# Kernel tuning notes

Hardware: AMD Instinct MI355X
Metric: run time of the kernel (lower is better)

Reference implementation:

```python
import jax, jax.numpy as jnp
import numpy as np

N = 50000          # nodes
E = 800000         # edges (before self-loops)
IN_CH = 128
HID = 64
HEADS = 4
OUT_CH = 16
NEG_SLOPE = 0.2    # PyG GATConv default leaky_relu slope
EPS = 1e-16        # PyG softmax denominator epsilon


def glorot(key, shape):
    fan_in, fan_out = shape[0], shape[-1]
    lim = np.sqrt(6.0 / (fan_in + fan_out))
    return jax.random.uniform(key, shape, jnp.float32, -lim, lim)


def setup_inputs() -> dict:
    key = jax.random.key(0)
    ks = jax.random.split(key, 12)
    x = jax.random.normal(ks[0], (N, IN_CH), jnp.float32)
    edge_index = jax.random.randint(ks[1], (2, E), 0, N, jnp.int32)
    # layer 1: in -> HID per head, HEADS heads
    W1 = glorot(ks[2], (IN_CH, HEADS * HID))
    a_src1 = glorot(ks[3], (HEADS, HID))
    a_dst1 = glorot(ks[4], (HEADS, HID))
    b1 = jnp.zeros((HEADS * HID,), jnp.float32)
    # layer 2: HEADS*HID -> OUT_CH, 1 head
    W2 = glorot(ks[5], (HEADS * HID, OUT_CH))
    a_src2 = glorot(ks[6], (1, OUT_CH))
    a_dst2 = glorot(ks[7], (1, OUT_CH))
    b2 = jnp.zeros((OUT_CH,), jnp.float32)
    return {"x": x, "edge_index": edge_index,
            "W1": W1, "a_src1": a_src1, "a_dst1": a_dst1, "b1": b1,
            "W2": W2, "a_src2": a_src2, "a_dst2": a_dst2, "b2": b2}


def gat_conv(x, edge_index, W, a_src, a_dst, b, heads, ch):
    """PyG GATConv: linear, edge attention, segment softmax over dst, scatter-agg."""
    n = x.shape[0]
    loops = jnp.arange(n, dtype=edge_index.dtype)
    src = jnp.concatenate([edge_index[0], loops])   # add_self_loops=True
    dst = jnp.concatenate([edge_index[1], loops])
    h = (x @ W).reshape(n, heads, ch)               # [N, H, C]
    s_src = jnp.einsum('nhc,hc->nh', h, a_src)      # [N, H]
    s_dst = jnp.einsum('nhc,hc->nh', h, a_dst)
    e = s_src[src] + s_dst[dst]                     # [E', H]
    e = jnp.where(e > 0, e, NEG_SLOPE * e)          # leaky_relu
    m = jax.ops.segment_max(e, dst, num_segments=n)  # per-dst max
    ex = jnp.exp(e - m[dst])
    denom = jax.ops.segment_sum(ex, dst, num_segments=n)
    alpha = ex / (denom[dst] + EPS)                 # [E', H]
    out = jax.ops.segment_sum(h[src] * alpha[:, :, None], dst, num_segments=n)
    return out.reshape(n, heads * ch) + b


def reference(x, edge_index, W1, a_src1, a_dst1, b1, W2, a_src2, a_dst2, b2):
    h = gat_conv(x, edge_index, W1, a_src1, a_dst1, b1, HEADS, HID)
    h = jax.nn.elu(h)
    return gat_conv(h, edge_index, W2, a_src2, a_dst2, b2, 1, OUT_CH)
```

## Files before the change

kernel.cpp:

```cpp
#include <hip/hip_runtime.h>
#include <cstdint>
#include <cstddef>

#define NN 50000
#define IN_CH 128
#define C1 256
#define HID 64
#define HEADS 4
#define OUT_CH 16
#define NEG_SLOPE 0.2f
#define EPS_SM 1e-16f
#define NEGINF -3.4e38f
#define NBUK ((NN + 255) >> 8)

typedef __attribute__((ext_vector_type(8))) short bf16x8;
typedef __attribute__((ext_vector_type(4))) float f32x4;

__device__ __forceinline__ unsigned short f2b(float f) {
    unsigned int u = __float_as_uint(f);
    u += 0x7fffu + ((u >> 16) & 1u);
    return (unsigned short)(u >> 16);
}
__device__ __forceinline__ float b2f_lo(unsigned int packed) {
    return __uint_as_float(packed << 16);
}
__device__ __forceinline__ float b2f_hi(unsigned int packed) {
    return __uint_as_float(packed & 0xffff0000u);
}

__global__ void cvt_weights(const float* __restrict__ W1, const float* __restrict__ W2,
                            const float* __restrict__ a_src1, const float* __restrict__ a_dst1,
                            unsigned short* __restrict__ w1t, unsigned short* __restrict__ w2b,
                            unsigned short* __restrict__ waSDt) {
    int b = blockIdx.x, t = threadIdx.x;
    if (b < 128) {
        w1t[t * 128 + b] = f2b(W1[b * 256 + t]);
    } else if (b < 144) {
        int k = (b - 128) * 16 + (t >> 4);
        int c = t & 15;
        w2b[c * 256 + k] = f2b(W2[k * 16 + c]);
    } else {
        if (t < 128) {
            const float* wrow = W1 + t * 256;
#pragma unroll
            for (int h = 0; h < 4; ++h) {
                float ss = 0.f, sd = 0.f;
#pragma unroll
                for (int c = 0; c < 64; ++c) {
                    float w = wrow[h * 64 + c];
                    ss += w * a_src1[h * 64 + c];
                    sd += w * a_dst1[h * 64 + c];
                }
                waSDt[h * 128 + t] = f2b(ss);
                waSDt[(4 + h) * 128 + t] = f2b(sd);
            }
#pragma unroll
            for (int c = 8; c < 16; ++c) waSDt[c * 128 + t] = 0;
        }
    }
}

__global__ __launch_bounds__(256) void gemm1_mfma(const float* __restrict__ X,
                                                  const unsigned short* __restrict__ w1t,
                                                  const unsigned short* __restrict__ waSDt,
                                                  unsigned short* __restrict__ h1b,
                                                  float* __restrict__ ssrc1,
                                                  float* __restrict__ sdst1, int M) {
    __shared__ unsigned short xb[64 * 128];
    __shared__ unsigned short wt[256 * 128];
    int tid = threadIdx.x;
    int m0 = blockIdx.x * 64;
    {
        const uint4* gp = (const uint4*)w1t;
#pragma unroll
        for (int r = 0; r < 16; ++r) {
            int idx = r * 256 + tid;
            int byte = idx * 16;
            int row = byte >> 8;
            int cb = byte & 255;
            uint4 v = gp[idx];
            *(uint4*)((char*)wt + row * 256 + (cb ^ ((row & 7) << 4))) = v;
        }
    }
    {
#pragma unroll
        for (int r = 0; r < 8; ++r) {
            int f = r * 256 + tid;
            int e = f * 4;
            int row = e >> 7, col = e & 127;
            float4 v = make_float4(0.f, 0.f, 0.f, 0.f);
            if (m0 + row < M) v = *(const float4*)&X[(size_t)(m0 + row) * 128 + col];
            ushort4 bb;
            bb.x = f2b(v.x); bb.y = f2b(v.y); bb.z = f2b(v.z); bb.w = f2b(v.w);
            *(ushort4*)((char*)xb + row * 256 + ((col * 2) ^ ((row & 7) << 4))) = bb;
        }
    }
    __syncthreads();
    int wv = tid >> 6, l = tid & 63;
    int lm = l & 15, lk = l >> 4;
    int swz = (lm & 7) << 4;
    bf16x8 sfr[4];
#pragma unroll
    for (int kk = 0; kk < 4; ++kk)
        sfr[kk] = *(const bf16x8*)&waSDt[lm * 128 + kk * 32 + lk * 8];
    f32x4 acc[4][4];
    f32x4 accS[4];
#pragma unroll
    for (int a = 0; a < 4; ++a) {
        accS[a] = (f32x4){0.f, 0.f, 0.f, 0.f};
#pragma unroll
        for (int b = 0; b < 4; ++b) acc[a][b] = (f32x4){0.f, 0.f, 0.f, 0.f};
    }
#pragma unroll
    for (int kk = 0; kk < 4; ++kk) {
        int kb = (kk * 64 + lk * 16) ^ swz;
        bf16x8 af[4], bfr[4];
#pragma unroll
        for (int mf = 0; mf < 4; ++mf)
            af[mf] = *(const bf16x8*)((const char*)xb + (mf * 16 + lm) * 256 + kb);
#pragma unroll
        for (int nt = 0; nt < 4; ++nt)
            bfr[nt] = *(const bf16x8*)((const char*)wt + (wv * 64 + nt * 16 + lm) * 256 + kb);
#pragma unroll
        for (int mf = 0; mf < 4; ++mf) {
#pragma unroll
            for (int nt = 0; nt < 4; ++nt)
                acc[mf][nt] = __builtin_amdgcn_mfma_f32_16x16x32_bf16(af[mf], bfr[nt], acc[mf][nt], 0, 0, 0);
            accS[mf] = __builtin_amdgcn_mfma_f32_16x16x32_bf16(af[mf], sfr[kk], accS[mf], 0, 0, 0);
        }
    }
#pragma unroll
    for (int mf = 0; mf < 4; ++mf) {
#pragma unroll
        for (int r = 0; r < 4; ++r) {
            int row = m0 + mf * 16 + lk * 4 + r;
            if (row < M) {
#pragma unroll
                for (int nt = 0; nt < 4; ++nt)
                    h1b[(size_t)row * 256 + wv * 64 + nt * 16 + lm] = f2b(acc[mf][nt][r]);
            }
        }
    }
    {
        f32x4 as = accS[wv];
#pragma unroll
        for (int r = 0; r < 4; ++r) {
            int row = m0 + wv * 16 + lk * 4 + r;
            if (row < M && lm < 8) {
                if (lm < 4) ssrc1[row * HEADS + lm] = as[r];
                else        sdst1[row * HEADS + (lm - 4)] = as[r];
            }
        }
    }
}

__global__ __launch_bounds__(256) void bucket_count(const int* __restrict__ dst_arr,
                                                    int* __restrict__ bcount,
                                                    int Etot, int E) {
    __shared__ int cnt[NBUK];
    int t = threadIdx.x;
    for (int i = t; i < NBUK; i += 256) cnt[i] = 0;
    __syncthreads();
    for (int i = blockIdx.x * 256 + t; i < Etot; i += gridDim.x * 256) {
        int dst = (i < E) ? dst_arr[i] : (i - E);
        atomicAdd(&cnt[dst >> 8], 1);
    }
    __syncthreads();
    for (int i = t; i < NBUK; i += 256)
        if (cnt[i]) atomicAdd(&bcount[i], cnt[i]);
}

__global__ __launch_bounds__(256) void bucket_scan(const int* __restrict__ bcount,
                                                   int* __restrict__ bbase,
                                                   int* __restrict__ bcursor,
                                                   int* __restrict__ rowst, int Etot) {
    __shared__ int s[256];
    int t = threadIdx.x;
    int x = (t < NBUK) ? bcount[t] : 0;
    s[t] = x;
    __syncthreads();
    for (int off = 1; off < 256; off <<= 1) {
        int v = (t >= off) ? s[t - off] : 0;
        __syncthreads();
        s[t] += v;
        __syncthreads();
    }
    int excl = s[t] - x;
    if (t < NBUK) {
        bbase[t] = excl;
        bcursor[t] = excl;
    }
    if (t == 0) {
        bbase[NBUK] = Etot;
        rowst[NN] = Etot;
    }
}

__global__ __launch_bounds__(256) void bucket_scatter(const int* __restrict__ src_arr,
                                                      const int* __restrict__ dst_arr,
                                                      int* __restrict__ bcursor,
                                                      unsigned int* __restrict__ ebuf,
                                                      int Etot, int E) {
    __shared__ int cnt[NBUK];
    __shared__ int cur[NBUK];
    int t = threadIdx.x;
    for (int i = t; i < NBUK; i += 256) cnt[i] = 0;
    __syncthreads();
    for (int i = blockIdx.x * 256 + t; i < Etot; i += gridDim.x * 256) {
        int dst = (i < E) ? dst_arr[i] : (i - E);
        atomicAdd(&cnt[dst >> 8], 1);
    }
    __syncthreads();
    for (int i = t; i < NBUK; i += 256)
        cur[i] = cnt[i] ? atomicAdd(&bcursor[i], cnt[i]) : 0;
    __syncthreads();
    for (int i = blockIdx.x * 256 + t; i < Etot; i += gridDim.x * 256) {
        int dst, src;
        if (i < E) { dst = dst_arr[i]; src = src_arr[i]; }
        else { dst = i - E; src = i - E; }
        int pos = atomicAdd(&cur[dst >> 8], 1);
        ebuf[pos] = ((unsigned int)(dst & 255) << 16) | (unsigned int)src;
    }
}

__global__ __launch_bounds__(256) void bucket_csr(const unsigned int* __restrict__ ebuf,
                                                  const int* __restrict__ bbase,
                                                  int* __restrict__ rowst,
                                                  int* __restrict__ srcs) {
    __shared__ int sdeg[256];
    __shared__ int scur[256];
    int t = threadIdx.x, b = blockIdx.x;
    int ebase = bbase[b], eend = bbase[b + 1];
    sdeg[t] = 0;
    __syncthreads();
    for (int i = ebase + t; i < eend; i += 256)
        atomicAdd(&sdeg[ebuf[i] >> 16], 1);
    __syncthreads();
    int x = sdeg[t];
    __syncthreads();
    for (int off = 1; off < 256; off <<= 1) {
        int v = (t >= off) ? sdeg[t - off] : 0;
        __syncthreads();
        sdeg[t] += v;
        __syncthreads();
    }
    int excl = sdeg[t] - x;
    int gnode = b * 256 + t;
    if (gnode < NN) rowst[gnode] = ebase + excl;
    scur[t] = excl;
    __syncthreads();
    for (int i = ebase + t; i < eend; i += 256) {
        unsigned int e = ebuf[i];
        int pos = atomicAdd(&scur[e >> 16], 1);
        srcs[ebase + pos] = (int)(e & 0xffffu);
    }
}

__global__ __launch_bounds__(256) void agg1_fused(const unsigned short* __restrict__ h1b,
                                                  const float* __restrict__ ssrc1,
                                                  const float* __restrict__ sdst1,
                                                  const int* __restrict__ row_start,
                                                  const int* __restrict__ srcs,
                                                  const float* __restrict__ b1,
                                                  unsigned short* __restrict__ out1b) {
    __shared__ float alds[4][64][4];
    int wid = threadIdx.x >> 6;
    int d = blockIdx.x * 4 + wid;
    int l = threadIdx.x & 63;
    int start = row_start[d], end = row_start[d + 1];
    int deg = end - start;

    int sub = l & 15, h = l >> 4;
    float sdstA = sdst1[d * HEADS + h];
    auto comp = [&](int i) -> float {
        int s = srcs[i];
        float e = ssrc1[s * HEADS + h] + sdstA;
        return e > 0.f ? e : NEG_SLOPE * e;
    };
    float e0 = NEGINF, e1 = NEGINF, e2 = NEGINF, e3 = NEGINF;
    int i0 = start + sub;
    if (i0 < end) e0 = comp(i0);
    if (i0 + 16 < end) e1 = comp(i0 + 16);
    if (i0 + 32 < end) e2 = comp(i0 + 32);
    if (i0 + 48 < end) e3 = comp(i0 + 48);
    float mx = fmaxf(fmaxf(e0, e1), fmaxf(e2, e3));
    for (int i = i0 + 64; i < end; i += 16) mx = fmaxf(mx, comp(i));
#pragma unroll
    for (int o = 1; o < 16; o <<= 1) mx = fmaxf(mx, __shfl_xor(mx, o));
    float s0 = __expf(e0 - mx), s1 = __expf(e1 - mx);
    float s2 = __expf(e2 - mx), s3 = __expf(e3 - mx);
    float ssum = s0 + s1 + s2 + s3;
    for (int i = i0 + 64; i < end; i += 16) ssum += __expf(comp(i) - mx);
#pragma unroll
    for (int o = 1; o < 16; o <<= 1) ssum += __shfl_xor(ssum, o);
    float inv = 1.f / (ssum + EPS_SM);
    alds[wid][sub][h] = s0 * inv;
    alds[wid][sub + 16][h] = s1 * inv;
    alds[wid][sub + 32][h] = s2 * inv;
    alds[wid][sub + 48][h] = s3 * inv;

    int half = l >> 5;
    int cl = l & 31;
    int hc = cl >> 3;
    const int cb = cl * 8;
    float acc[8] = {};
    int i = start + half;
    if (deg <= 64) {
        for (; i + 6 < end; i += 8) {
            int s0_ = srcs[i], s1_ = srcs[i + 2], s2_ = srcs[i + 4], s3_ = srcs[i + 6];
            uint4 v0 = *(const uint4*)&h1b[(size_t)s0_ * C1 + cb];
            uint4 v1 = *(const uint4*)&h1b[(size_t)s1_ * C1 + cb];
            uint4 v2 = *(const uint4*)&h1b[(size_t)s2_ * C1 + cb];
            uint4 v3 = *(const uint4*)&h1b[(size_t)s3_ * C1 + cb];
            float a0 = alds[wid][i - start][hc];
            float a1 = alds[wid][i + 2 - start][hc];
            float a2 = alds[wid][i + 4 - start][hc];
            float a3 = alds[wid][i + 6 - start][hc];
            acc[0] += a0 * b2f_lo(v0.x) + a1 * b2f_lo(v1.x) + a2 * b2f_lo(v2.x) + a3 * b2f_lo(v3.x);
            acc[1] += a0 * b2f_hi(v0.x) + a1 * b2f_hi(v1.x) + a2 * b2f_hi(v2.x) + a3 * b2f_hi(v3.x);
            acc[2] += a0 * b2f_lo(v0.y) + a1 * b2f_lo(v1.y) + a2 * b2f_lo(v2.y) + a3 * b2f_lo(v3.y);
            acc[3] += a0 * b2f_hi(v0.y) + a1 * b2f_hi(v1.y) + a2 * b2f_hi(v2.y) + a3 * b2f_hi(v3.y);
            acc[4] += a0 * b2f_lo(v0.z) + a1 * b2f_lo(v1.z) + a2 * b2f_lo(v2.z) + a3 * b2f_lo(v3.z);
            acc[5] += a0 * b2f_hi(v0.z) + a1 * b2f_hi(v1.z) + a2 * b2f_hi(v2.z) + a3 * b2f_hi(v3.z);
            acc[6] += a0 * b2f_lo(v0.w) + a1 * b2f_lo(v1.w) + a2 * b2f_lo(v2.w) + a3 * b2f_lo(v3.w);
            acc[7] += a0 * b2f_hi(v0.w) + a1 * b2f_hi(v1.w) + a2 * b2f_hi(v2.w) + a3 * b2f_hi(v3.w);
        }
        for (; i < end; i += 2) {
            int s = srcs[i];
            uint4 v = *(const uint4*)&h1b[(size_t)s * C1 + cb];
            float a = alds[wid][i - start][hc];
            acc[0] += a * b2f_lo(v.x); acc[1] += a * b2f_hi(v.x);
            acc[2] += a * b2f_lo(v.y); acc[3] += a * b2f_hi(v.y);
            acc[4] += a * b2f_lo(v.z); acc[5] += a * b2f_hi(v.z);
            acc[6] += a * b2f_lo(v.w); acc[7] += a * b2f_hi(v.w);
        }
    } else {
        float mxB = __shfl(mx, hc << 4);
        float invB = __shfl(inv, hc << 4);
        float sdstB = __shfl(sdstA, hc << 4);
        for (; i < end; i += 2) {
            int s = srcs[i];
            uint4 v = *(const uint4*)&h1b[(size_t)s * C1 + cb];
            float e = ssrc1[s * HEADS + hc] + sdstB;
            e = e > 0.f ? e : NEG_SLOPE * e;
            float a = __expf(e - mxB) * invB;
            acc[0] += a * b2f_lo(v.x); acc[1] += a * b2f_hi(v.x);
            acc[2] += a * b2f_lo(v.y); acc[3] += a * b2f_hi(v.y);
            acc[4] += a * b2f_lo(v.z); acc[5] += a * b2f_hi(v.z);
            acc[6] += a * b2f_lo(v.w); acc[7] += a * b2f_hi(v.w);
        }
    }
#pragma unroll
    for (int j = 0; j < 8; ++j) acc[j] += __shfl_xor(acc[j], 32);
    if (half == 0) {
        float4 ba = *(const float4*)&b1[cb];
        float4 bbv = *(const float4*)&b1[cb + 4];
        float v[8];
        v[0] = acc[0] + ba.x;  v[1] = acc[1] + ba.y;
        v[2] = acc[2] + ba.z;  v[3] = acc[3] + ba.w;
        v[4] = acc[4] + bbv.x; v[5] = acc[5] + bbv.y;
        v[6] = acc[6] + bbv.z; v[7] = acc[7] + bbv.w;
        bf16x8 o;
#pragma unroll
        for (int j = 0; j < 8; ++j) {
            float t = v[j] > 0.f ? v[j] : (__expf(v[j]) - 1.f);
            o[j] = (short)f2b(t);
        }
        *(bf16x8*)&out1b[(size_t)d * C1 + cb] = o;
    }
}

__global__ __launch_bounds__(256) void gemm2_mfma(const unsigned short* __restrict__ out1b,
                                                  const unsigned short* __restrict__ w2b,
                                                  const float* __restrict__ a_src2,
                                                  const float* __restrict__ a_dst2,
                                                  float* __restrict__ h2,
                                                  float* __restrict__ ssrc2,
                                                  float* __restrict__ sdst2, int M) {
    __shared__ char ab[64 * 528];
    int tid = threadIdx.x;
    int m0 = blockIdx.x * 64;
#pragma unroll
    for (int r = 0; r < 8; ++r) {
        int byte = r * 4096 + tid * 16;
        int row = byte >> 9, col = byte & 511;
        uint4 v = make_uint4(0u, 0u, 0u, 0u);
        if (m0 + row < M)
            v = *(const uint4*)((const char*)out1b + (size_t)(m0 + row) * 512 + col);
        *(uint4*)(ab + row * 528 + col) = v;
    }
    int wv = tid >> 6, l = tid & 63;
    int lm = l & 15, lk = l >> 4;
    bf16x8 bfr[8];
#pragma unroll
    for (int kk = 0; kk < 8; ++kk)
        bfr[kk] = *(const bf16x8*)&w2b[lm * 256 + lk * 8 + kk * 32];
    __syncthreads();
    f32x4 acc = (f32x4){0.f, 0.f, 0.f, 0.f};
    const char* base = ab + (wv * 16 + lm) * 528 + lk * 16;
#pragma unroll
    for (int kk = 0; kk < 8; ++kk) {
        bf16x8 af = *(const bf16x8*)(base + kk * 64);
        acc = __builtin_amdgcn_mfma_f32_16x16x32_bf16(af, bfr[kk], acc, 0, 0, 0);
    }
    float asc = a_src2[lm], adc = a_dst2[lm];
#pragma unroll
    for (int r = 0; r < 4; ++r) {
        int grow = m0 + wv * 16 + lk * 4 + r;
        float v = acc[r];
        float ps = v * asc, pd = v * adc;
#pragma unroll
        for (int o = 1; o < 16; o <<= 1) {
            ps += __shfl_xor(ps, o);
            pd += __shfl_xor(pd, o);
        }
        if (grow < M) {
            h2[(size_t)grow * OUT_CH + lm] = v;
            if (lm == 0) {
                ssrc2[grow] = ps;
                sdst2[grow] = pd;
            }
        }
    }
}

__global__ __launch_bounds__(256) void agg2_fused(const float* __restrict__ h2,
                                                  const float* __restrict__ ssrc2,
                                                  const float* __restrict__ sdst2,
                                                  const int* __restrict__ row_start,
                                                  const int* __restrict__ srcs,
                                                  const float* __restrict__ b2,
                                                  float* __restrict__ out) {
    __shared__ float alds[4][128];
    int wid = threadIdx.x >> 6;
    int d = blockIdx.x * 4 + wid;
    int l = threadIdx.x & 63;
    int start = row_start[d], end = row_start[d + 1];
    int deg = end - start;
    float sdst = sdst2[d];
    auto comp = [&](int i) -> float {
        int s = srcs[i];
        float e = ssrc2[s] + sdst;
        return e > 0.f ? e : NEG_SLOPE * e;
    };
    float e0 = NEGINF, e1 = NEGINF;
    int i0 = start + l;
    if (i0 < end) e0 = comp(i0);
    if (i0 + 64 < end) e1 = comp(i0 + 64);
    float mx = fmaxf(e0, e1);
    for (int i = i0 + 128; i < end; i += 64) mx = fmaxf(mx, comp(i));
#pragma unroll
    for (int o = 1; o < 64; o <<= 1) mx = fmaxf(mx, __shfl_xor(mx, o));
    float s0 = __expf(e0 - mx), s1 = __expf(e1 - mx);
    float ssum = s0 + s1;
    for (int i = i0 + 128; i < end; i += 64) ssum += __expf(comp(i) - mx);
#pragma unroll
    for (int o = 1; o < 64; o <<= 1) ssum += __shfl_xor(ssum, o);
    float inv = 1.f / (ssum + EPS_SM);
    alds[wid][l] = s0 * inv;
    alds[wid][l + 64] = s1 * inv;

    int slot = l >> 2;
    int c4 = (l & 3) * 4;
    float4 acc = make_float4(0.f, 0.f, 0.f, 0.f);
    if (deg <= 128) {
        for (int i = start + slot; i < end; i += 16) {
            int s = srcs[i];
            float a = alds[wid][i - start];
            float4 v = *(const float4*)&h2[(size_t)s * OUT_CH + c4];
            acc.x += a * v.x; acc.y += a * v.y; acc.z += a * v.z; acc.w += a * v.w;
        }
    } else {
        for (int i = start + slot; i < end; i += 16) {
            int s = srcs[i];
            float e = ssrc2[s] + sdst;
            e = e > 0.f ? e : NEG_SLOPE * e;
            float a = __expf(e - mx) * inv;
            float4 v = *(const float4*)&h2[(size_t)s * OUT_CH + c4];
            acc.x += a * v.x; acc.y += a * v.y; acc.z += a * v.z; acc.w += a * v.w;
        }
    }
#pragma unroll
    for (int o = 4; o < 64; o <<= 1) {
        acc.x += __shfl_xor(acc.x, o);
        acc.y += __shfl_xor(acc.y, o);
        acc.z += __shfl_xor(acc.z, o);
        acc.w += __shfl_xor(acc.w, o);
    }
    if (l < 4) {
        float4 bb = *(const float4*)&b2[c4];
        float4 r = make_float4(acc.x + bb.x, acc.y + bb.y, acc.z + bb.z, acc.w + bb.w);
        *(float4*)&out[(size_t)d * OUT_CH + c4] = r;
    }
}

extern "C" void kernel_launch(void* const* d_in, const int* in_sizes, int n_in,
                              void* d_out, int out_size, void* d_ws, size_t ws_size,
                              hipStream_t stream) {
    const float* x      = (const float*)d_in[0];
    const int*   ei     = (const int*)d_in[1];
    const float* W1     = (const float*)d_in[2];
    const float* a_src1 = (const float*)d_in[3];
    const float* a_dst1 = (const float*)d_in[4];
    const float* b1     = (const float*)d_in[5];
    const float* W2     = (const float*)d_in[6];
    const float* a_src2 = (const float*)d_in[7];
    const float* a_dst2 = (const float*)d_in[8];
    const float* b2     = (const float*)d_in[9];
    float* out = (float*)d_out;

    const int E = in_sizes[1] / 2;
    const int Etot = E + NN;
    const int* src_arr = ei;
    const int* dst_arr = ei + E;

    size_t off = 0;
    auto carve = [&](size_t bytes) -> void* {
        void* r = (char*)d_ws + off;
        off += (bytes + 255) & ~(size_t)255;
        return r;
    };
    unsigned short* h1b  = (unsigned short*)carve((size_t)NN * C1 * 2);
    unsigned short* out1b= (unsigned short*)carve((size_t)NN * C1 * 2);
    unsigned short* w1t  = (unsigned short*)carve((size_t)IN_CH * C1 * 2);
    unsigned short* w2b  = (unsigned short*)carve((size_t)C1 * OUT_CH * 2);
    unsigned short* waSDt= (unsigned short*)carve((size_t)16 * 128 * 2);
    float* ssrc1 = (float*)carve((size_t)NN * HEADS * 4);
    float* sdst1 = (float*)carve((size_t)NN * HEADS * 4);
    float* h2    = (float*)carve((size_t)NN * OUT_CH * 4);
    float* ssrc2 = (float*)carve((size_t)NN * 4);
    float* sdst2 = (float*)carve((size_t)NN * 4);
    int* rowst   = (int*)carve((size_t)(NN + 1) * 4);
    int* srcs    = (int*)carve((size_t)Etot * 4);
    unsigned int* ebuf = (unsigned int*)carve((size_t)Etot * 4);
    int* bcount  = (int*)carve((size_t)NBUK * 4);
    int* bbase   = (int*)carve((size_t)(NBUK + 1) * 4);
    int* bcursor = (int*)carve((size_t)NBUK * 4);

    hipMemsetAsync(bcount, 0, (size_t)NBUK * 4, stream);
    bucket_count<<<256, 256, 0, stream>>>(dst_arr, bcount, Etot, E);
    bucket_scan<<<1, 256, 0, stream>>>(bcount, bbase, bcursor, rowst, Etot);
    bucket_scatter<<<256, 256, 0, stream>>>(src_arr, dst_arr, bcursor, ebuf, Etot, E);
    bucket_csr<<<NBUK, 256, 0, stream>>>(ebuf, bbase, rowst, srcs);

    cvt_weights<<<145, 256, 0, stream>>>(W1, W2, a_src1, a_dst1, w1t, w2b, waSDt);

    gemm1_mfma<<<(NN + 63) / 64, 256, 0, stream>>>(x, w1t, waSDt, h1b, ssrc1, sdst1, NN);
    agg1_fused<<<NN / 4, 256, 0, stream>>>(h1b, ssrc1, sdst1, rowst, srcs, b1, out1b);

    gemm2_mfma<<<(NN + 63) / 64, 256, 0, stream>>>(out1b, w2b, a_src2, a_dst2,
                                                   h2, ssrc2, sdst2, NN);
    agg2_fused<<<NN / 4, 256, 0, stream>>>(h2, ssrc2, sdst2, rowst, srcs, b2, out);
}
```

Before: 171.6 us.

## Fuse layer-2 linear projection into layer-1 aggregation and drop W1 LDS staging

```diff
diff --git a/kernel.cpp b/kernel.cpp
--- a/kernel.cpp
+++ b/kernel.cpp
@@ -67,21 +67,8 @@
                                                   float* __restrict__ ssrc1,
                                                   float* __restrict__ sdst1, int M) {
     __shared__ unsigned short xb[64 * 128];
-    __shared__ unsigned short wt[256 * 128];
     int tid = threadIdx.x;
     int m0 = blockIdx.x * 64;
-    {
-        const uint4* gp = (const uint4*)w1t;
-#pragma unroll
-        for (int r = 0; r < 16; ++r) {
-            int idx = r * 256 + tid;
-            int byte = idx * 16;
-            int row = byte >> 8;
-            int cb = byte & 255;
-            uint4 v = gp[idx];
-            *(uint4*)((char*)wt + row * 256 + (cb ^ ((row & 7) << 4))) = v;
-        }
-    }
     {
 #pragma unroll
         for (int r = 0; r < 8; ++r) {
@@ -120,7 +107,7 @@
             af[mf] = *(const bf16x8*)((const char*)xb + (mf * 16 + lm) * 256 + kb);
 #pragma unroll
         for (int nt = 0; nt < 4; ++nt)
-            bfr[nt] = *(const bf16x8*)((const char*)wt + (wv * 64 + nt * 16 + lm) * 256 + kb);
+            bfr[nt] = *(const bf16x8*)&w1t[(wv * 64 + nt * 16 + lm) * 128 + kk * 32 + lk * 8];
 #pragma unroll
         for (int mf = 0; mf < 4; ++mf) {
 #pragma unroll
@@ -262,7 +249,12 @@
                                                   const int* __restrict__ row_start,
                                                   const int* __restrict__ srcs,
                                                   const float* __restrict__ b1,
-                                                  unsigned short* __restrict__ out1b) {
+                                                  const unsigned short* __restrict__ w2b,
+                                                  const float* __restrict__ a_src2,
+                                                  const float* __restrict__ a_dst2,
+                                                  float* __restrict__ h2,
+                                                  float* __restrict__ ssrc2,
+                                                  float* __restrict__ sdst2) {
     __shared__ float alds[4][64][4];
     int wid = threadIdx.x >> 6;
     int d = blockIdx.x * 4 + wid;
@@ -352,74 +344,43 @@
     }
 #pragma unroll
     for (int j = 0; j < 8; ++j) acc[j] += __shfl_xor(acc[j], 32);
-    if (half == 0) {
-        float4 ba = *(const float4*)&b1[cb];
-        float4 bbv = *(const float4*)&b1[cb + 4];
-        float v[8];
-        v[0] = acc[0] + ba.x;  v[1] = acc[1] + ba.y;
-        v[2] = acc[2] + ba.z;  v[3] = acc[3] + ba.w;
-        v[4] = acc[4] + bbv.x; v[5] = acc[5] + bbv.y;
-        v[6] = acc[6] + bbv.z; v[7] = acc[7] + bbv.w;
-        bf16x8 o;
-#pragma unroll
-        for (int j = 0; j < 8; ++j) {
-            float t = v[j] > 0.f ? v[j] : (__expf(v[j]) - 1.f);
-            o[j] = (short)f2b(t);
-        }
-        *(bf16x8*)&out1b[(size_t)d * C1 + cb] = o;
-    }
-}
-
-__global__ __launch_bounds__(256) void gemm2_mfma(const unsigned short* __restrict__ out1b,
-                                                  const unsigned short* __restrict__ w2b,
-                                                  const float* __restrict__ a_src2,
-                                                  const float* __restrict__ a_dst2,
-                                                  float* __restrict__ h2,
-                                                  float* __restrict__ ssrc2,
-                                                  float* __restrict__ sdst2, int M) {
-    __shared__ char ab[64 * 528];
-    int tid = threadIdx.x;
-    int m0 = blockIdx.x * 64;
-#pragma unroll
-    for (int r = 0; r < 8; ++r) {
-        int byte = r * 4096 + tid * 16;
-        int row = byte >> 9, col = byte & 511;
-        uint4 v = make_uint4(0u, 0u, 0u, 0u);
-        if (m0 + row < M)
-            v = *(const uint4*)((const char*)out1b + (size_t)(m0 + row) * 512 + col);
-        *(uint4*)(ab + row * 528 + col) = v;
-    }
-    int wv = tid >> 6, l = tid & 63;
+
+    float4 ba = *(const float4*)&b1[cb];
+    float4 bbv = *(const float4*)&b1[cb + 4];
+    float v[8];
+    v[0] = acc[0] + ba.x;  v[1] = acc[1] + ba.y;
+    v[2] = acc[2] + ba.z;  v[3] = acc[3] + ba.w;
+    v[4] = acc[4] + bbv.x; v[5] = acc[5] + bbv.y;
+    v[6] = acc[6] + bbv.z; v[7] = acc[7] + bbv.w;
+#pragma unroll
+    for (int j = 0; j < 8; ++j) v[j] = v[j] > 0.f ? v[j] : (__expf(v[j]) - 1.f);
+    unsigned int pk[4];
+#pragma unroll
+    for (int q = 0; q < 4; ++q)
+        pk[q] = (unsigned int)f2b(v[2 * q]) | ((unsigned int)f2b(v[2 * q + 1]) << 16);
     int lm = l & 15, lk = l >> 4;
-    bf16x8 bfr[8];
-#pragma unroll
-    for (int kk = 0; kk < 8; ++kk)
-        bfr[kk] = *(const bf16x8*)&w2b[lm * 256 + lk * 8 + kk * 32];
-    __syncthreads();
-    f32x4 acc = (f32x4){0.f, 0.f, 0.f, 0.f};
-    const char* base = ab + (wv * 16 + lm) * 528 + lk * 16;
-#pragma unroll
-    for (int kk = 0; kk < 8; ++kk) {
-        bf16x8 af = *(const bf16x8*)(base + kk * 64);
-        acc = __builtin_amdgcn_mfma_f32_16x16x32_bf16(af, bfr[kk], acc, 0, 0, 0);
-    }
-    float asc = a_src2[lm], adc = a_dst2[lm];
-#pragma unroll
-    for (int r = 0; r < 4; ++r) {
-        int grow = m0 + wv * 16 + lk * 4 + r;
-        float v = acc[r];
-        float ps = v * asc, pd = v * adc;
-#pragma unroll
-        for (int o = 1; o < 16; o <<= 1) {
-            ps += __shfl_xor(ps, o);
-            pd += __shfl_xor(pd, o);
-        }
-        if (grow < M) {
-            h2[(size_t)grow * OUT_CH + lm] = v;
-            if (lm == 0) {
-                ssrc2[grow] = ps;
-                sdst2[grow] = pd;
-            }
+    f32x4 accH = (f32x4){0.f, 0.f, 0.f, 0.f};
+#pragma unroll
+    for (int t = 0; t < 8; ++t) {
+        bf16x8 afr = *(const bf16x8*)&w2b[lm * 256 + t * 32 + lk * 8];
+        int srcl = t * 4 + lk;
+        union { unsigned int u[4]; bf16x8 b; } bu;
+#pragma unroll
+        for (int q = 0; q < 4; ++q) bu.u[q] = (unsigned int)__shfl((int)pk[q], srcl);
+        accH = __builtin_amdgcn_mfma_f32_16x16x32_bf16(afr, bu.b, accH, 0, 0, 0);
+    }
+    if (lm == 0) {
+        float4 hv = make_float4(accH[0], accH[1], accH[2], accH[3]);
+        *(float4*)&h2[(size_t)d * OUT_CH + lk * 4] = hv;
+        float4 as2 = *(const float4*)&a_src2[lk * 4];
+        float4 ad2 = *(const float4*)&a_dst2[lk * 4];
+        float ps = hv.x * as2.x + hv.y * as2.y + hv.z * as2.z + hv.w * as2.w;
+        float pd = hv.x * ad2.x + hv.y * ad2.y + hv.z * ad2.z + hv.w * ad2.w;
+        ps += __shfl_xor(ps, 16); ps += __shfl_xor(ps, 32);
+        pd += __shfl_xor(pd, 16); pd += __shfl_xor(pd, 32);
+        if (lk == 0) {
+            ssrc2[d] = ps;
+            sdst2[d] = pd;
         }
     }
 }
@@ -458,7 +419,7 @@
     for (int o = 1; o < 64; o <<= 1) ssum += __shfl_xor(ssum, o);
     float inv = 1.f / (ssum + EPS_SM);
     alds[wid][l] = s0 * inv;
-    alds[wid][l + 64] = s1 * inv;
+    if (l + 64 < 128) alds[wid][l + 64] = s1 * inv;
 
     int slot = l >> 2;
     int c4 = (l & 3) * 4;
@@ -521,7 +482,6 @@
         return r;
     };
     unsigned short* h1b  = (unsigned short*)carve((size_t)NN * C1 * 2);
-    unsigned short* out1b= (unsigned short*)carve((size_t)NN * C1 * 2);
     unsigned short* w1t  = (unsigned short*)carve((size_t)IN_CH * C1 * 2);
     unsigned short* w2b  = (unsigned short*)carve((size_t)C1 * OUT_CH * 2);
     unsigned short* waSDt= (unsigned short*)carve((size_t)16 * 128 * 2);
@@ -546,9 +506,8 @@
     cvt_weights<<<145, 256, 0, stream>>>(W1, W2, a_src1, a_dst1, w1t, w2b, waSDt);
 
     gemm1_mfma<<<(NN + 63) / 64, 256, 0, stream>>>(x, w1t, waSDt, h1b, ssrc1, sdst1, NN);
-    agg1_fused<<<NN / 4, 256, 0, stream>>>(h1b, ssrc1, sdst1, rowst, srcs, b1, out1b);
-
-    gemm2_mfma<<<(NN + 63) / 64, 256, 0, stream>>>(out1b, w2b, a_src2, a_dst2,
-                                                   h2, ssrc2, sdst2, NN);
+    agg1_fused<<<NN / 4, 256, 0, stream>>>(h1b, ssrc1, sdst1, rowst, srcs, b1,
+                                           w2b, a_src2, a_dst2, h2, ssrc2, sdst2);
+
     agg2_fused<<<NN / 4, 256, 0, stream>>>(h2, ssrc2, sdst2, rowst, srcs, b2, out);
 }
```

Result: slower. 187.0 us (+9.0%).

## Split layer-1 aggregation into alpha pass and channel-sliced gather; drop W1 LDS staging

Applied to the files above, without the earlier changes.

```diff
diff --git a/kernel.cpp b/kernel.cpp
--- a/kernel.cpp
+++ b/kernel.cpp
@@ -67,21 +67,8 @@
                                                   float* __restrict__ ssrc1,
                                                   float* __restrict__ sdst1, int M) {
     __shared__ unsigned short xb[64 * 128];
-    __shared__ unsigned short wt[256 * 128];
     int tid = threadIdx.x;
     int m0 = blockIdx.x * 64;
-    {
-        const uint4* gp = (const uint4*)w1t;
-#pragma unroll
-        for (int r = 0; r < 16; ++r) {
-            int idx = r * 256 + tid;
-            int byte = idx * 16;
-            int row = byte >> 8;
-            int cb = byte & 255;
-            uint4 v = gp[idx];
-            *(uint4*)((char*)wt + row * 256 + (cb ^ ((row & 7) << 4))) = v;
-        }
-    }
     {
 #pragma unroll
         for (int r = 0; r < 8; ++r) {
@@ -120,7 +107,7 @@
             af[mf] = *(const bf16x8*)((const char*)xb + (mf * 16 + lm) * 256 + kb);
 #pragma unroll
         for (int nt = 0; nt < 4; ++nt)
-            bfr[nt] = *(const bf16x8*)((const char*)wt + (wv * 64 + nt * 16 + lm) * 256 + kb);
+            bfr[nt] = *(const bf16x8*)&w1t[(wv * 64 + nt * 16 + lm) * 128 + kk * 32 + lk * 8];
 #pragma unroll
         for (int mf = 0; mf < 4; ++mf) {
 #pragma unroll
@@ -256,25 +243,19 @@
     }
 }
 
-__global__ __launch_bounds__(256) void agg1_fused(const unsigned short* __restrict__ h1b,
-                                                  const float* __restrict__ ssrc1,
-                                                  const float* __restrict__ sdst1,
-                                                  const int* __restrict__ row_start,
-                                                  const int* __restrict__ srcs,
-                                                  const float* __restrict__ b1,
-                                                  unsigned short* __restrict__ out1b) {
-    __shared__ float alds[4][64][4];
-    int wid = threadIdx.x >> 6;
-    int d = blockIdx.x * 4 + wid;
+__global__ __launch_bounds__(256) void agg1a_kernel(const float* __restrict__ ssrc1,
+                                                    const float* __restrict__ sdst1,
+                                                    const int* __restrict__ row_start,
+                                                    const int* __restrict__ srcs,
+                                                    float* __restrict__ alpha1h, int Etot) {
+    int d = blockIdx.x * 4 + (threadIdx.x >> 6);
     int l = threadIdx.x & 63;
+    int sub = l & 15, h = l >> 4;
     int start = row_start[d], end = row_start[d + 1];
-    int deg = end - start;
-
-    int sub = l & 15, h = l >> 4;
-    float sdstA = sdst1[d * HEADS + h];
+    float sdst = sdst1[d * HEADS + h];
     auto comp = [&](int i) -> float {
         int s = srcs[i];
-        float e = ssrc1[s * HEADS + h] + sdstA;
+        float e = ssrc1[s * HEADS + h] + sdst;
         return e > 0.f ? e : NEG_SLOPE * e;
     };
     float e0 = NEGINF, e1 = NEGINF, e2 = NEGINF, e3 = NEGINF;
@@ -294,67 +275,52 @@
 #pragma unroll
     for (int o = 1; o < 16; o <<= 1) ssum += __shfl_xor(ssum, o);
     float inv = 1.f / (ssum + EPS_SM);
-    alds[wid][sub][h] = s0 * inv;
-    alds[wid][sub + 16][h] = s1 * inv;
-    alds[wid][sub + 32][h] = s2 * inv;
-    alds[wid][sub + 48][h] = s3 * inv;
-
-    int half = l >> 5;
-    int cl = l & 31;
-    int hc = cl >> 3;
-    const int cb = cl * 8;
+    float* ah = alpha1h + (size_t)h * Etot;
+    if (i0 < end) ah[i0] = s0 * inv;
+    if (i0 + 16 < end) ah[i0 + 16] = s1 * inv;
+    if (i0 + 32 < end) ah[i0 + 32] = s2 * inv;
+    if (i0 + 48 < end) ah[i0 + 48] = s3 * inv;
+    for (int i = i0 + 64; i < end; i += 16) ah[i] = __expf(comp(i) - mx) * inv;
+}
+
+__global__ __launch_bounds__(256) void agg1b_slice(const unsigned short* __restrict__ h1b,
+                                                   const float* __restrict__ alpha1h,
+                                                   const int* __restrict__ row_start,
+                                                   const int* __restrict__ srcs,
+                                                   const float* __restrict__ b1,
+                                                   unsigned short* __restrict__ out1b,
+                                                   int Etot) {
+    int wg = blockIdx.x;
+    int slice = wg & 7;
+    int grp = wg >> 3;
+    int wid = threadIdx.x >> 6;
+    int d = grp * 4 + wid;
+    int l = threadIdx.x & 63;
+    int slot = l >> 2, c4 = l & 3;
+    int start = row_start[d], end = row_start[d + 1];
+    const int cb = slice * 32 + c4 * 8;
+    const float* ah = alpha1h + (size_t)(slice >> 1) * Etot;
     float acc[8] = {};
-    int i = start + half;
-    if (deg <= 64) {
-        for (; i + 6 < end; i += 8) {
-            int s0_ = srcs[i], s1_ = srcs[i + 2], s2_ = srcs[i + 4], s3_ = srcs[i + 6];
-            uint4 v0 = *(const uint4*)&h1b[(size_t)s0_ * C1 + cb];
-            uint4 v1 = *(const uint4*)&h1b[(size_t)s1_ * C1 + cb];
-            uint4 v2 = *(const uint4*)&h1b[(size_t)s2_ * C1 + cb];
-            uint4 v3 = *(const uint4*)&h1b[(size_t)s3_ * C1 + cb];
-            float a0 = alds[wid][i - start][hc];
-            float a1 = alds[wid][i + 2 - start][hc];
-            float a2 = alds[wid][i + 4 - start][hc];
-            float a3 = alds[wid][i + 6 - start][hc];
-            acc[0] += a0 * b2f_lo(v0.x) + a1 * b2f_lo(v1.x) + a2 * b2f_lo(v2.x) + a3 * b2f_lo(v3.x);
-            acc[1] += a0 * b2f_hi(v0.x) + a1 * b2f_hi(v1.x) + a2 * b2f_hi(v2.x) + a3 * b2f_hi(v3.x);
-            acc[2] += a0 * b2f_lo(v0.y) + a1 * b2f_lo(v1.y) + a2 * b2f_lo(v2.y) + a3 * b2f_lo(v3.y);
-            acc[3] += a0 * b2f_hi(v0.y) + a1 * b2f_hi(v1.y) + a2 * b2f_hi(v2.y) + a3 * b2f_hi(v3.y);
-            acc[4] += a0 * b2f_lo(v0.z) + a1 * b2f_lo(v1.z) + a2 * b2f_lo(v2.z) + a3 * b2f_lo(v3.z);
-            acc[5] += a0 * b2f_hi(v0.z) + a1 * b2f_hi(v1.z) + a2 * b2f_hi(v2.z) + a3 * b2f_hi(v3.z);
-            acc[6] += a0 * b2f_lo(v0.w) + a1 * b2f_lo(v1.w) + a2 * b2f_lo(v2.w) + a3 * b2f_lo(v3.w);
-            acc[7] += a0 * b2f_hi(v0.w) + a1 * b2f_hi(v1.w) + a2 * b2f_hi(v2.w) + a3 * b2f_hi(v3.w);
-        }
-        for (; i < end; i += 2) {
-            int s = srcs[i];
-            uint4 v = *(const uint4*)&h1b[(size_t)s * C1 + cb];
-            float a = alds[wid][i - start][hc];
-            acc[0] += a * b2f_lo(v.x); acc[1] += a * b2f_hi(v.x);
-            acc[2] += a * b2f_lo(v.y); acc[3] += a * b2f_hi(v.y);
-            acc[4] += a * b2f_lo(v.z); acc[5] += a * b2f_hi(v.z);
-            acc[6] += a * b2f_lo(v.w); acc[7] += a * b2f_hi(v.w);
-        }
-    } else {
-        float mxB = __shfl(mx, hc << 4);
-        float invB = __shfl(inv, hc << 4);
-        float sdstB = __shfl(sdstA, hc << 4);
-        for (; i < end; i += 2) {
-            int s = srcs[i];
-            uint4 v = *(const uint4*)&h1b[(size_t)s * C1 + cb];
-            float e = ssrc1[s * HEADS + hc] + sdstB;
-            e = e > 0.f ? e : NEG_SLOPE * e;
-            float a = __expf(e - mxB) * invB;
-            acc[0] += a * b2f_lo(v.x); acc[1] += a * b2f_hi(v.x);
-            acc[2] += a * b2f_lo(v.y); acc[3] += a * b2f_hi(v.y);
-            acc[4] += a * b2f_lo(v.z); acc[5] += a * b2f_hi(v.z);
-            acc[6] += a * b2f_lo(v.w); acc[7] += a * b2f_hi(v.w);
-        }
-    }
-#pragma unroll
-    for (int j = 0; j < 8; ++j) acc[j] += __shfl_xor(acc[j], 32);
-    if (half == 0) {
-        float4 ba = *(const float4*)&b1[cb];
-        float4 bbv = *(const float4*)&b1[cb + 4];
+    for (int i = start + slot; i < end; i += 16) {
+        int s = srcs[i];
+        float a = ah[i];
+        uint4 v = *(const uint4*)&h1b[(size_t)s * C1 + cb];
+        acc[0] += a * b2f_lo(v.x); acc[1] += a * b2f_hi(v.x);
+        acc[2] += a * b2f_lo(v.y); acc[3] += a * b2f_hi(v.y);
+        acc[4] += a * b2f_lo(v.z); acc[5] += a * b2f_hi(v.z);
+        acc[6] += a * b2f_lo(v.w); acc[7] += a * b2f_hi(v.w);
+    }
+#pragma unroll
+    for (int j = 0; j < 8; ++j) {
+        acc[j] += __shfl_xor(acc[j], 4);
+        acc[j] += __shfl_xor(acc[j], 8);
+        acc[j] += __shfl_xor(acc[j], 16);
+        acc[j] += __shfl_xor(acc[j], 32);
+    }
+    if (l < 4) {
+        int cbase = slice * 32 + l * 8;
+        float4 ba = *(const float4*)&b1[cbase];
+        float4 bbv = *(const float4*)&b1[cbase + 4];
         float v[8];
         v[0] = acc[0] + ba.x;  v[1] = acc[1] + ba.y;
         v[2] = acc[2] + ba.z;  v[3] = acc[3] + ba.w;
@@ -366,7 +332,7 @@
             float t = v[j] > 0.f ? v[j] : (__expf(v[j]) - 1.f);
             o[j] = (short)f2b(t);
         }
-        *(bf16x8*)&out1b[(size_t)d * C1 + cb] = o;
+        *(bf16x8*)&out1b[(size_t)d * C1 + cbase] = o;
     }
 }
 
@@ -530,6 +496,7 @@
     float* h2    = (float*)carve((size_t)NN * OUT_CH * 4);
     float* ssrc2 = (float*)carve((size_t)NN * 4);
     float* sdst2 = (float*)carve((size_t)NN * 4);
+    float* alpha1h = (float*)carve((size_t)HEADS * Etot * 4);
     int* rowst   = (int*)carve((size_t)(NN + 1) * 4);
     int* srcs    = (int*)carve((size_t)Etot * 4);
     unsigned int* ebuf = (unsigned int*)carve((size_t)Etot * 4);
@@ -546,7 +513,8 @@
     cvt_weights<<<145, 256, 0, stream>>>(W1, W2, a_src1, a_dst1, w1t, w2b, waSDt);
 
     gemm1_mfma<<<(NN + 63) / 64, 256, 0, stream>>>(x, w1t, waSDt, h1b, ssrc1, sdst1, NN);
-    agg1_fused<<<NN / 4, 256, 0, stream>>>(h1b, ssrc1, sdst1, rowst, srcs, b1, out1b);
+    agg1a_kernel<<<NN / 4, 256, 0, stream>>>(ssrc1, sdst1, rowst, srcs, alpha1h, Etot);
+    agg1b_slice<<<(NN / 4) * 8, 256, 0, stream>>>(h1b, alpha1h, rowst, srcs, b1, out1b, Etot);
 
     gemm2_mfma<<<(NN + 63) / 64, 256, 0, stream>>>(out1b, w2b, a_src2, a_dst2,
                                                    h2, ssrc2, sdst2, NN);
```

Result: slower. 279.8 us (+63.1%).

## Fuse independent CSR-build and weight/GEMM1 kernels via block-range partitioning

Applied to the files above, without the earlier changes.

```diff
diff --git a/kernel.cpp b/kernel.cpp
--- a/kernel.cpp
+++ b/kernel.cpp
@@ -12,6 +12,7 @@
 #define EPS_SM 1e-16f
 #define NEGINF -3.4e38f
 #define NBUK ((NN + 255) >> 8)
+#define NGEMM1 ((NN + 63) / 64)
 
 typedef __attribute__((ext_vector_type(8))) short bf16x8;
 typedef __attribute__((ext_vector_type(4))) float f32x4;
@@ -28,146 +29,56 @@
     return __uint_as_float(packed & 0xffff0000u);
 }
 
-__global__ void cvt_weights(const float* __restrict__ W1, const float* __restrict__ W2,
-                            const float* __restrict__ a_src1, const float* __restrict__ a_dst1,
-                            unsigned short* __restrict__ w1t, unsigned short* __restrict__ w2b,
-                            unsigned short* __restrict__ waSDt) {
-    int b = blockIdx.x, t = threadIdx.x;
-    if (b < 128) {
-        w1t[t * 128 + b] = f2b(W1[b * 256 + t]);
-    } else if (b < 144) {
-        int k = (b - 128) * 16 + (t >> 4);
-        int c = t & 15;
-        w2b[c * 256 + k] = f2b(W2[k * 16 + c]);
-    } else {
-        if (t < 128) {
-            const float* wrow = W1 + t * 256;
-#pragma unroll
-            for (int h = 0; h < 4; ++h) {
-                float ss = 0.f, sd = 0.f;
-#pragma unroll
-                for (int c = 0; c < 64; ++c) {
-                    float w = wrow[h * 64 + c];
-                    ss += w * a_src1[h * 64 + c];
-                    sd += w * a_dst1[h * 64 + c];
-                }
-                waSDt[h * 128 + t] = f2b(ss);
-                waSDt[(4 + h) * 128 + t] = f2b(sd);
-            }
-#pragma unroll
-            for (int c = 8; c < 16; ++c) waSDt[c * 128 + t] = 0;
-        }
-    }
-}
-
-__global__ __launch_bounds__(256) void gemm1_mfma(const float* __restrict__ X,
-                                                  const unsigned short* __restrict__ w1t,
-                                                  const unsigned short* __restrict__ waSDt,
-                                                  unsigned short* __restrict__ h1b,
-                                                  float* __restrict__ ssrc1,
-                                                  float* __restrict__ sdst1, int M) {
-    __shared__ unsigned short xb[64 * 128];
-    __shared__ unsigned short wt[256 * 128];
-    int tid = threadIdx.x;
-    int m0 = blockIdx.x * 64;
-    {
-        const uint4* gp = (const uint4*)w1t;
-#pragma unroll
-        for (int r = 0; r < 16; ++r) {
-            int idx = r * 256 + tid;
-            int byte = idx * 16;
-            int row = byte >> 8;
-            int cb = byte & 255;
-            uint4 v = gp[idx];
-            *(uint4*)((char*)wt + row * 256 + (cb ^ ((row & 7) << 4))) = v;
-        }
-    }
-    {
-#pragma unroll
-        for (int r = 0; r < 8; ++r) {
-            int f = r * 256 + tid;
-            int e = f * 4;
-            int row = e >> 7, col = e & 127;
-            float4 v = make_float4(0.f, 0.f, 0.f, 0.f);
-            if (m0 + row < M) v = *(const float4*)&X[(size_t)(m0 + row) * 128 + col];
-            ushort4 bb;
-            bb.x = f2b(v.x); bb.y = f2b(v.y); bb.z = f2b(v.z); bb.w = f2b(v.w);
-            *(ushort4*)((char*)xb + row * 256 + ((col * 2) ^ ((row & 7) << 4))) = bb;
-        }
-    }
-    __syncthreads();
-    int wv = tid >> 6, l = tid & 63;
-    int lm = l & 15, lk = l >> 4;
-    int swz = (lm & 7) << 4;
-    bf16x8 sfr[4];
-#pragma unroll
-    for (int kk = 0; kk < 4; ++kk)
-        sfr[kk] = *(const bf16x8*)&waSDt[lm * 128 + kk * 32 + lk * 8];
-    f32x4 acc[4][4];
-    f32x4 accS[4];
-#pragma unroll
-    for (int a = 0; a < 4; ++a) {
-        accS[a] = (f32x4){0.f, 0.f, 0.f, 0.f};
-#pragma unroll
-        for (int b = 0; b < 4; ++b) acc[a][b] = (f32x4){0.f, 0.f, 0.f, 0.f};
-    }
-#pragma unroll
-    for (int kk = 0; kk < 4; ++kk) {
-        int kb = (kk * 64 + lk * 16) ^ swz;
-        bf16x8 af[4], bfr[4];
-#pragma unroll
-        for (int mf = 0; mf < 4; ++mf)
-            af[mf] = *(const bf16x8*)((const char*)xb + (mf * 16 + lm) * 256 + kb);
-#pragma unroll
-        for (int nt = 0; nt < 4; ++nt)
-            bfr[nt] = *(const bf16x8*)((const char*)wt + (wv * 64 + nt * 16 + lm) * 256 + kb);
-#pragma unroll
-        for (int mf = 0; mf < 4; ++mf) {
-#pragma unroll
-            for (int nt = 0; nt < 4; ++nt)
-                acc[mf][nt] = __builtin_amdgcn_mfma_f32_16x16x32_bf16(af[mf], bfr[nt], acc[mf][nt], 0, 0, 0);
-            accS[mf] = __builtin_amdgcn_mfma_f32_16x16x32_bf16(af[mf], sfr[kk], accS[mf], 0, 0, 0);
-        }
-    }
-#pragma unroll
-    for (int mf = 0; mf < 4; ++mf) {
-#pragma unroll
-        for (int r = 0; r < 4; ++r) {
-            int row = m0 + mf * 16 + lk * 4 + r;
-            if (row < M) {
-#pragma unroll
-                for (int nt = 0; nt < 4; ++nt)
-                    h1b[(size_t)row * 256 + wv * 64 + nt * 16 + lm] = f2b(acc[mf][nt][r]);
-            }
-        }
-    }
-    {
-        f32x4 as = accS[wv];
-#pragma unroll
-        for (int r = 0; r < 4; ++r) {
-            int row = m0 + wv * 16 + lk * 4 + r;
-            if (row < M && lm < 8) {
-                if (lm < 4) ssrc1[row * HEADS + lm] = as[r];
-                else        sdst1[row * HEADS + (lm - 4)] = as[r];
-            }
-        }
-    }
-}
-
-__global__ __launch_bounds__(256) void bucket_count(const int* __restrict__ dst_arr,
-                                                    int* __restrict__ bcount,
-                                                    int Etot, int E) {
+__global__ __launch_bounds__(256) void fused_count_cvt(const int* __restrict__ dst_arr,
+                                                       int* __restrict__ bcount,
+                                                       int Etot, int E,
+                                                       const float* __restrict__ W1,
+                                                       const float* __restrict__ W2,
+                                                       const float* __restrict__ a_src1,
+                                                       const float* __restrict__ a_dst1,
+                                                       unsigned short* __restrict__ w1t,
+                                                       unsigned short* __restrict__ w2b,
+                                                       unsigned short* __restrict__ waSDt) {
     __shared__ int cnt[NBUK];
     int t = threadIdx.x;
-    for (int i = t; i < NBUK; i += 256) cnt[i] = 0;
-    __syncthreads();
-    for (int i = blockIdx.x * 256 + t; i < Etot; i += gridDim.x * 256) {
-        int dst = (i < E) ? dst_arr[i] : (i - E);
-        atomicAdd(&cnt[dst >> 8], 1);
-    }
-    __syncthreads();
-    for (int i = t; i < NBUK; i += 256)
-        if (cnt[i]) atomicAdd(&bcount[i], cnt[i]);
+    if (blockIdx.x < 256) {
+        for (int i = t; i < NBUK; i += 256) cnt[i] = 0;
+        __syncthreads();
+        for (int i = blockIdx.x * 256 + t; i < Etot; i += 65536) {
+            int dst = (i < E) ? dst_arr[i] : (i - E);
+            atomicAdd(&cnt[dst >> 8], 1);
+        }
+        __syncthreads();
+        for (int i = t; i < NBUK; i += 256)
+            if (cnt[i]) atomicAdd(&bcount[i], cnt[i]);
+    } else {
+        int b = blockIdx.x - 256;
+        if (b < 128) {
+            w1t[t * 128 + b] = f2b(W1[b * 256 + t]);
+        } else if (b < 144) {
+            int k = (b - 128) * 16 + (t >> 4);
+            int c = t & 15;
+            w2b[c * 256 + k] = f2b(W2[k * 16 + c]);
+        } else {
+            if (t < 128) {
+                const float* wrow = W1 + t * 256;
+#pragma unroll
+                for (int h = 0; h < 4; ++h) {
+                    float ss = 0.f, sd = 0.f;
+#pragma unroll
+                    for (int c = 0; c < 64; ++c) {
+                        float w = wrow[h * 64 + c];
+                        ss += w * a_src1[h * 64 + c];
+                        sd += w * a_dst1[h * 64 + c];
+                    }
+                    waSDt[h * 128 + t] = f2b(ss);
+                    waSDt[(4 + h) * 128 + t] = f2b(sd);
+                }
+#pragma unroll
+                for (int c = 8; c < 16; ++c) waSDt[c * 128 + t] = 0;
+            }
+        }
+    }
 }
 
 __global__ __launch_bounds__(256) void bucket_scan(const int* __restrict__ bcount,
@@ -196,30 +107,110 @@
     }
 }
 
-__global__ __launch_bounds__(256) void bucket_scatter(const int* __restrict__ src_arr,
-                                                      const int* __restrict__ dst_arr,
-                                                      int* __restrict__ bcursor,
-                                                      unsigned int* __restrict__ ebuf,
-                                                      int Etot, int E) {
+__global__ __launch_bounds__(256) void fused_gemm1_scatter(
+        const float* __restrict__ X,
+        const unsigned short* __restrict__ w1t,
+        const unsigned short* __restrict__ waSDt,
+        unsigned short* __restrict__ h1b,
+        float* __restrict__ ssrc1,
+        float* __restrict__ sdst1, int M,
+        const int* __restrict__ src_arr, const int* __restrict__ dst_arr,
+        int* __restrict__ bcursor, unsigned int* __restrict__ ebuf,
+        int Etot, int E) {
+    __shared__ unsigned short xb[64 * 128];
     __shared__ int cnt[NBUK];
     __shared__ int cur[NBUK];
-    int t = threadIdx.x;
-    for (int i = t; i < NBUK; i += 256) cnt[i] = 0;
-    __syncthreads();
-    for (int i = blockIdx.x * 256 + t; i < Etot; i += gridDim.x * 256) {
-        int dst = (i < E) ? dst_arr[i] : (i - E);
-        atomicAdd(&cnt[dst >> 8], 1);
-    }
-    __syncthreads();
-    for (int i = t; i < NBUK; i += 256)
-        cur[i] = cnt[i] ? atomicAdd(&bcursor[i], cnt[i]) : 0;
-    __syncthreads();
-    for (int i = blockIdx.x * 256 + t; i < Etot; i += gridDim.x * 256) {
-        int dst, src;
-        if (i < E) { dst = dst_arr[i]; src = src_arr[i]; }
-        else { dst = i - E; src = i - E; }
-        int pos = atomicAdd(&cur[dst >> 8], 1);
-        ebuf[pos] = ((unsigned int)(dst & 255) << 16) | (unsigned int)src;
+    int tid = threadIdx.x;
+    if (blockIdx.x < NGEMM1) {
+        int m0 = blockIdx.x * 64;
+#pragma unroll
+        for (int r = 0; r < 8; ++r) {
+            int f = r * 256 + tid;
+            int e = f * 4;
+            int row = e >> 7, col = e & 127;
+            float4 v = make_float4(0.f, 0.f, 0.f, 0.f);
+            if (m0 + row < M) v = *(const float4*)&X[(size_t)(m0 + row) * 128 + col];
+            ushort4 bb;
+            bb.x = f2b(v.x); bb.y = f2b(v.y); bb.z = f2b(v.z); bb.w = f2b(v.w);
+            *(ushort4*)((char*)xb + row * 256 + ((col * 2) ^ ((row & 7) << 4))) = bb;
+        }
+        __syncthreads();
+        int wv = tid >> 6, l = tid & 63;
+        int lm = l & 15, lk = l >> 4;
+        int swz = (lm & 7) << 4;
+        bf16x8 sfr[4];
+#pragma unroll
+        for (int kk = 0; kk < 4; ++kk)
+            sfr[kk] = *(const bf16x8*)&waSDt[lm * 128 + kk * 32 + lk * 8];
+        f32x4 acc[4][4];
+        f32x4 accS[4];
+#pragma unroll
+        for (int a = 0; a < 4; ++a) {
+            accS[a] = (f32x4){0.f, 0.f, 0.f, 0.f};
+#pragma unroll
+            for (int b = 0; b < 4; ++b) acc[a][b] = (f32x4){0.f, 0.f, 0.f, 0.f};
+        }
+#pragma unroll
+        for (int kk = 0; kk < 4; ++kk) {
+            int kb = (kk * 64 + lk * 16) ^ swz;
+            bf16x8 af[4], bfr[4];
+#pragma unroll
+            for (int mf = 0; mf < 4; ++mf)
+                af[mf] = *(const bf16x8*)((const char*)xb + (mf * 16 + lm) * 256 + kb);
+#pragma unroll
+            for (int nt = 0; nt < 4; ++nt)
+                bfr[nt] = *(const bf16x8*)&w1t[(wv * 64 + nt * 16 + lm) * 128 + kk * 32 + lk * 8];
+#pragma unroll
+            for (int mf = 0; mf < 4; ++mf) {
+#pragma unroll
+                for (int nt = 0; nt < 4; ++nt)
+                    acc[mf][nt] = __builtin_amdgcn_mfma_f32_16x16x32_bf16(af[mf], bfr[nt], acc[mf][nt], 0, 0, 0);
+                accS[mf] = __builtin_amdgcn_mfma_f32_16x16x32_bf16(af[mf], sfr[kk], accS[mf], 0, 0, 0);
+            }
+        }
+#pragma unroll
+        for (int mf = 0; mf < 4; ++mf) {
+#pragma unroll
+            for (int r = 0; r < 4; ++r) {
+                int row = m0 + mf * 16 + lk * 4 + r;
+                if (row < M) {
+#pragma unroll
+                    for (int nt = 0; nt < 4; ++nt)
+                        h1b[(size_t)row * 256 + wv * 64 + nt * 16 + lm] = f2b(acc[mf][nt][r]);
+                }
+            }
+        }
+        {
+            f32x4 as = accS[wv];
+#pragma unroll
+            for (int r = 0; r < 4; ++r) {
+                int row = m0 + wv * 16 + lk * 4 + r;
+                if (row < M && lm < 8) {
+                    if (lm < 4) ssrc1[row * HEADS + lm] = as[r];
+                    else        sdst1[row * HEADS + (lm - 4)] = as[r];
+                }
+            }
+        }
+    } else {
+        int bid = blockIdx.x - NGEMM1;
+        int t = tid;
+        for (int i = t; i < NBUK; i += 256) cnt[i] = 0;
+        __syncthreads();
+        for (int i = bid * 256 + t; i < Etot; i += 65536) {
+            int dst = (i < E) ? dst_arr[i] : (i - E);
+            atomicAdd(&cnt[dst >> 8], 1);
+        }
+        __syncthreads();
+        for (int i = t; i < NBUK; i += 256)
+            cur[i] = cnt[i] ? atomicAdd(&bcursor[i], cnt[i]) : 0;
+        __syncthreads();
+        for (int i = bid * 256 + t; i < Etot; i += 65536) {
+            int dst, src;
+            if (i < E) { dst = dst_arr[i]; src = src_arr[i]; }
+            else { dst = i - E; src = i - E; }
+            int pos = atomicAdd(&cur[dst >> 8], 1);
+            ebuf[pos] = ((unsigned int)(dst & 255) << 16) | (unsigned int)src;
+        }
     }
 }
 
@@ -538,17 +529,17 @@
     int* bcursor = (int*)carve((size_t)NBUK * 4);
 
     hipMemsetAsync(bcount, 0, (size_t)NBUK * 4, stream);
-    bucket_count<<<256, 256, 0, stream>>>(dst_arr, bcount, Etot, E);
+    fused_count_cvt<<<256 + 145, 256, 0, stream>>>(dst_arr, bcount, Etot, E,
+                                                   W1, W2, a_src1, a_dst1,
+                                                   w1t, w2b, waSDt);
     bucket_scan<<<1, 256, 0, stream>>>(bcount, bbase, bcursor, rowst, Etot);
-    bucket_scatter<<<256, 256, 0, stream>>>(src_arr, dst_arr, bcursor, ebuf, Etot, E);
+    fused_gemm1_scatter<<<NGEMM1 + 256, 256, 0, stream>>>(x, w1t, waSDt,
+                                                          h1b, ssrc1, sdst1, NN,
+                                                          src_arr, dst_arr,
+                                                          bcursor, ebuf, Etot, E);
     bucket_csr<<<NBUK, 256, 0, stream>>>(ebuf, bbase, rowst, srcs);
-
-    cvt_weights<<<145, 256, 0, stream>>>(W1, W2, a_src1, a_dst1, w1t, w2b, waSDt);
-
-    gemm1_mfma<<<(NN + 63) / 64, 256, 0, stream>>>(x, w1t, waSDt, h1b, ssrc1, sdst1, NN);
     agg1_fused<<<NN / 4, 256, 0, stream>>>(h1b, ssrc1, sdst1, rowst, srcs, b1, out1b);
-
-    gemm2_mfma<<<(NN + 63) / 64, 256, 0, stream>>>(out1b, w2b, a_src2, a_dst2,
-                                                   h2, ssrc2, sdst2, NN);
+    gemm2_mfma<<<NGEMM1, 256, 0, stream>>>(out1b, w2b, a_src2, a_dst2,
+                                           h2, ssrc2, sdst2, NN);
     agg2_fused<<<NN / 4, 256, 0, stream>>>(h2, ssrc2, sdst2, rowst, srcs, b2, out);
 }
```

Result: faster. 164.4 us (-4.2%).
